# Kernel tuning notes

Measured on AMD Instinct MI355X. Metric: run time of the kernel, lower is better.

Reference implementation:

```python
import jax, jax.numpy as jnp
import numpy as np

B, T, E, H = 2, 2048, 1024, 16
Dh = E // H  # head_size = 64


def setup_inputs() -> dict:
    key = jax.random.key(0)
    ks = jax.random.split(key, 6)
    s = E ** -0.5
    x = jax.random.normal(ks[0], (B, T, E), dtype=jnp.float32)
    Wq = jax.random.normal(ks[1], (H, E, Dh), dtype=jnp.float32) * s
    Wk = jax.random.normal(ks[2], (H, E, Dh), dtype=jnp.float32) * s
    Wv = jax.random.normal(ks[3], (H, E, Dh), dtype=jnp.float32) * s
    wo_w = jax.random.normal(ks[4], (E, E), dtype=jnp.float32) * s  # torch Linear weight [out,in]
    wo_b = jax.random.normal(ks[5], (E,), dtype=jnp.float32) * 0.01
    return {"x": x, "Wq": Wq, "Wk": Wk, "Wv": Wv, "wo_w": wo_w, "wo_b": wo_b}


def reference(x, Wq, Wk, Wv, wo_w, wo_b):
    # Batched equivalent of the per-head Python loop: project all heads at once.
    q = jnp.einsum('bte,hed->bhtd', x, Wq)
    k = jnp.einsum('bte,hed->bhtd', x, Wk)
    v = jnp.einsum('bte,hed->bhtd', x, Wv)
    scale = Dh ** -0.5
    scores = jnp.einsum('bhtd,bhsd->bhts', q, k) * scale  # [B,H,T,T]
    causal = jnp.tril(jnp.ones((T, T), dtype=bool))
    scores = jnp.where(causal, scores, jnp.finfo(scores.dtype).min)
    att = jax.nn.softmax(scores, axis=-1)
    out = jnp.einsum('bhts,bhsd->bhtd', att, v)  # [B,H,T,Dh]
    # concat heads (head order along last dim, matching torch.cat over heads)
    out = out.transpose(0, 2, 1, 3).reshape(B, T, E)
    return out @ wo_w.T + wo_b
```

## Files before the change

kernel.cpp:

```cpp
#include <hip/hip_runtime.h>

#define B_ 2
#define T_ 2048
#define E_ 1024
#define H_ 16
#define DH 64

typedef unsigned short u16;
typedef unsigned int u32;
typedef __bf16 bf16x8 __attribute__((ext_vector_type(8)));
typedef float f32x4 __attribute__((ext_vector_type(4)));

__device__ __forceinline__ u16 f2bf(float f) {
  u32 u = __builtin_bit_cast(u32, f);
  u = u + 0x7FFFu + ((u >> 16) & 1u);
  return (u16)(u >> 16);
}
__device__ __forceinline__ float bf2f(u16 v) {
  return __builtin_bit_cast(float, (u32)v << 16);
}
__device__ __forceinline__ bf16x8 ldfrag(const u16* p) { return *(const bf16x8*)p; }

__device__ __forceinline__ void gload_lds16(const u16* g, u16* l) {
  __builtin_amdgcn_global_load_lds((const __attribute__((address_space(1))) u32*)g,
                                   (__attribute__((address_space(3))) u32*)l, 16, 0, 0);
}

__global__ __launch_bounds__(256) void k_conv_all(const float* __restrict__ x,
                                                  const float* __restrict__ Wq,
                                                  const float* __restrict__ Wk,
                                                  const float* __restrict__ Wv,
                                                  const float* __restrict__ wo_w,
                                                  u16* __restrict__ xb, u16* __restrict__ wT,
                                                  u16* __restrict__ woB) {
  __shared__ __align__(16) u16 Ls[64][68];
  const int t = threadIdx.x;
  const int bx = blockIdx.x;
  if (bx < 2048 || bx >= 2816) {
    const float* src = (bx < 2048) ? x : wo_w;
    u16* dst = (bx < 2048) ? xb : woB;
    u32 i = (((bx < 2048) ? bx : (bx - 2816)) * 256u + t) * 8u;
    float4 a = *(const float4*)(src + i);
    float4 b = *(const float4*)(src + i + 4);
    uint4 v;
    v.x = (u32)f2bf(a.x) | ((u32)f2bf(a.y) << 16);
    v.y = (u32)f2bf(a.z) | ((u32)f2bf(a.w) << 16);
    v.z = (u32)f2bf(b.x) | ((u32)f2bf(b.y) << 16);
    v.w = (u32)f2bf(b.z) | ((u32)f2bf(b.w) << 16);
    *(uint4*)(dst + i) = v;
    return;
  }
  const int idx = bx - 2048;
  const int e0 = (idx & 15) * 64;
  const int h = (idx >> 4) & 15;
  const int which = idx >> 8;
  const float* src = (which == 0) ? Wq : ((which == 1) ? Wk : Wv);
  const float scale = (which == 0) ? 0.18033688011112042f : 1.0f;
#pragma unroll
  for (int p = 0; p < 4; p++) {
    int id2 = p * 256 + t;
    int row = id2 >> 4, ch = id2 & 15;
    float4 v = *(const float4*)(src + ((size_t)h * E_ + e0 + row) * DH + ch * 4);
    uint2 pk;
    pk.x = (u32)f2bf(v.x * scale) | ((u32)f2bf(v.y * scale) << 16);
    pk.y = (u32)f2bf(v.z * scale) | ((u32)f2bf(v.w * scale) << 16);
    *(uint2*)(&Ls[row][ch * 4]) = pk;
  }
  __syncthreads();
  u16* dst = wT + ((size_t)which * H_ + h) * (DH * E_);
#pragma unroll
  for (int p = 0; p < 4; p++) {
    int id2 = p * 256 + t;
    int d = id2 >> 4, ec = id2 & 15;
    uint2 pk;
    pk.x = (u32)Ls[ec * 4 + 0][d] | ((u32)Ls[ec * 4 + 1][d] << 16);
    pk.y = (u32)Ls[ec * 4 + 2][d] | ((u32)Ls[ec * 4 + 3][d] << 16);
    *(uint2*)(dst + (size_t)d * E_ + e0 + ec * 4) = pk;
  }
}

__global__ __launch_bounds__(256, 3) void k_qkv(const u16* __restrict__ xb, const u16* __restrict__ wT,
                                                u16* __restrict__ Qb, u16* __restrict__ Kb,
                                                u16* __restrict__ VbT) {
  __shared__ __align__(16) u16 As[128 * 64];
  __shared__ __align__(16) u16 Bs[128 * 64];
  const int tid = threadIdx.x;
  const int w = tid >> 6, lane = tid & 63, quad = lane >> 4, lr = lane & 15;
  const int wr = w >> 1, wc = w & 1;
  const int t0 = blockIdx.x * 128;
  const int n0 = blockIdx.y * 128;
  const int sr = lane >> 3, sc = lane & 7;

  f32x4 acc[4][4];
  const f32x4 z4 = {0.f, 0.f, 0.f, 0.f};
#pragma unroll
  for (int i = 0; i < 4; i++)
#pragma unroll
    for (int j = 0; j < 4; j++) acc[i][j] = z4;

  for (int k0 = 0; k0 < E_; k0 += 64) {
    __syncthreads();
#pragma unroll
    for (int ii = 0; ii < 4; ii++) {
      int ra = w * 32 + ii * 8 + sr;
      gload_lds16(xb + (size_t)(t0 + ra) * E_ + k0 + ((sc ^ (ra & 7)) << 3),
                  As + (w * 32 + ii * 8) * 64);
      gload_lds16(wT + (size_t)(n0 + ra) * E_ + k0 + ((sc ^ (ra & 7)) << 3),
                  Bs + (w * 32 + ii * 8) * 64);
    }
    __syncthreads();
#pragma unroll
    for (int kk = 0; kk < 2; kk++) {
      bf16x8 af[4], bfv[4];
#pragma unroll
      for (int rt = 0; rt < 4; rt++) {
        int row = wr * 64 + rt * 16 + lr;
        af[rt] = ldfrag(As + row * 64 + (((kk * 4 + quad) ^ (row & 7)) << 3));
      }
#pragma unroll
      for (int ct = 0; ct < 4; ct++) {
        int row = wc * 64 + ct * 16 + lr;
        bfv[ct] = ldfrag(Bs + row * 64 + (((kk * 4 + quad) ^ (row & 7)) << 3));
      }
#pragma unroll
      for (int rt = 0; rt < 4; rt++)
#pragma unroll
        for (int ct = 0; ct < 4; ct++)
          acc[rt][ct] = __builtin_amdgcn_mfma_f32_16x16x32_bf16(af[rt], bfv[ct], acc[rt][ct], 0, 0, 0);
    }
  }

  const int qkv = n0 >> 10;
  if (qkv < 2) {
    u16* outp = (qkv == 0) ? Qb : Kb;
#pragma unroll
    for (int rt = 0; rt < 4; rt++)
#pragma unroll
      for (int ct = 0; ct < 4; ct++) {
        int n = n0 + wc * 64 + ct * 16 + lr;
        int h = (n >> 6) & 15, d = n & 63;
#pragma unroll
        for (int r = 0; r < 4; r++) {
          int t = t0 + wr * 64 + rt * 16 + quad * 4 + r;
          int bb = t >> 11, tt = t & 2047;
          outp[(((size_t)bb * H_ + h) * T_ + tt) * DH + d] = f2bf(acc[rt][ct][r]);
        }
      }
  } else {
#pragma unroll
    for (int rt = 0; rt < 4; rt++)
#pragma unroll
      for (int ct = 0; ct < 4; ct++) {
        int n = n0 + wc * 64 + ct * 16 + lr;
        int h = (n >> 6) & 15, d = n & 63;
        int t = t0 + wr * 64 + rt * 16 + quad * 4;
        int bb = t >> 11, tt = t & 2047;
        uint2 pk;
        pk.x = (u32)f2bf(acc[rt][ct][0]) | ((u32)f2bf(acc[rt][ct][1]) << 16);
        pk.y = (u32)f2bf(acc[rt][ct][2]) | ((u32)f2bf(acc[rt][ct][3]) << 16);
        *(uint2*)(VbT + (((size_t)bb * H_ + h) * DH + d) * T_ + tt) = pk;
      }
  }
}

__global__ __launch_bounds__(256, 6) void k_attn(const u16* __restrict__ Qb, const u16* __restrict__ Kb,
                                                 const u16* __restrict__ VbT, u16* __restrict__ O0,
                                                 u16* __restrict__ O1, u16* __restrict__ O2,
                                                 float* __restrict__ Lb) {
  __shared__ __align__(16) u16 Ks[4096];
  __shared__ __align__(16) u16 Vts[4096];
  __shared__ __align__(16) u16 Ps[4096];
  const int tid = threadIdx.x;
  const int w = tid >> 6, lane = tid & 63, quad = lane >> 4, lr = lane & 15;
  const int l7 = lr & 7;
  const int srow = lane >> 3, schunk = lane & 7;
  const int i = blockIdx.x / 3, s = blockIdx.x - 3 * i;
  const int h = blockIdx.y, bb = blockIdx.z;
  const u16* qb = Qb + ((size_t)bb * H_ + h) * (size_t)(T_ * DH);
  const u16* kb = Kb + ((size_t)bb * H_ + h) * (size_t)(T_ * DH);
  const u16* vbT = VbT + ((size_t)bb * H_ + h) * (size_t)(T_ * DH);
  const f32x4 z4 = {0.f, 0.f, 0.f, 0.f};
  const float MFIX = 20.0f;
  u16* const ops[3] = {O0, O1, O2};

  for (int jb = 0; jb < 2; jb++) {
    const int qt = jb ? i : (31 - i);
    const int t0 = qt * 64;

    const u16* qrow = qb + (size_t)(t0 + w * 16 + lr) * DH;
    bf16x8 bq0 = ldfrag(qrow + quad * 8);
    bf16x8 bq1 = ldfrag(qrow + 32 + quad * 8);

    f32x4 o_acc[4];
#pragma unroll
    for (int dt = 0; dt < 4; dt++) o_acc[dt] = z4;
    float l_i = 0.f;

    for (int jt = s; jt <= qt; jt += 3) {
      const int j0 = jt * 64;
      __syncthreads();
#pragma unroll
      for (int ii = 0; ii < 2; ii++) {
        int r = w * 16 + ii * 8 + srow;
        gload_lds16(kb + (size_t)(j0 + r) * DH + ((schunk ^ (r & 7)) << 3),
                    Ks + (w * 16 + ii * 8) * 64);
        gload_lds16(vbT + (size_t)r * T_ + j0 + ((schunk ^ (r & 7)) << 3),
                    Vts + (w * 16 + ii * 8) * 64);
      }
      __syncthreads();

      f32x4 s_acc[4];
#pragma unroll
      for (int st = 0; st < 4; st++) s_acc[st] = z4;
#pragma unroll
      for (int st = 0; st < 4; st++) {
        bf16x8 ak0 = ldfrag(Ks + (st * 16 + lr) * 64 + ((quad ^ l7) << 3));
        bf16x8 ak1 = ldfrag(Ks + (st * 16 + lr) * 64 + (((4 + quad) ^ l7) << 3));
        s_acc[st] = __builtin_amdgcn_mfma_f32_16x16x32_bf16(ak0, bq0, s_acc[st], 0, 0, 0);
        s_acc[st] = __builtin_amdgcn_mfma_f32_16x16x32_bf16(ak1, bq1, s_acc[st], 0, 0, 0);
      }

      if (jt == qt) {
        int qloc = w * 16 + lr;
#pragma unroll
        for (int st = 0; st < 4; st++) {
          int sbase = st * 16 + quad * 4;
#pragma unroll
          for (int r = 0; r < 4; r++)
            if (sbase + r > qloc) s_acc[st][r] = -__builtin_inff();
        }
      }

      float rsum = 0.f;
#pragma unroll
      for (int st = 0; st < 4; st++) {
        float p0 = __builtin_amdgcn_exp2f(s_acc[st][0] - MFIX);
        float p1 = __builtin_amdgcn_exp2f(s_acc[st][1] - MFIX);
        float p2 = __builtin_amdgcn_exp2f(s_acc[st][2] - MFIX);
        float p3 = __builtin_amdgcn_exp2f(s_acc[st][3] - MFIX);
        rsum += (p0 + p1) + (p2 + p3);
        uint2 pk;
        pk.x = (__builtin_bit_cast(u32, p0) >> 16) | (__builtin_bit_cast(u32, p1) & 0xffff0000u);
        pk.y = (__builtin_bit_cast(u32, p2) >> 16) | (__builtin_bit_cast(u32, p3) & 0xffff0000u);
        *(uint2*)(Ps + (w * 16 + lr) * 64 + (((st * 2 + (quad >> 1)) ^ l7) << 3) + ((quad & 1) << 2)) = pk;
      }
      l_i += rsum;

#pragma unroll
      for (int kk = 0; kk < 2; kk++) {
        bf16x8 bp = ldfrag(Ps + (w * 16 + lr) * 64 + (((kk * 4 + quad) ^ l7) << 3));
#pragma unroll
        for (int dt = 0; dt < 4; dt++) {
          bf16x8 av = ldfrag(Vts + (dt * 16 + lr) * 64 + (((kk * 4 + quad) ^ l7) << 3));
          o_acc[dt] = __builtin_amdgcn_mfma_f32_16x16x32_bf16(av, bp, o_acc[dt], 0, 0, 0);
        }
      }
    }

    l_i += __shfl_xor(l_i, 16);
    l_i += __shfl_xor(l_i, 32);

    u16* op = ops[s];
    int t = t0 + w * 16 + lr;
    u16* orow = op + ((size_t)bb * T_ + t) * E_ + h * DH;
#pragma unroll
    for (int dt = 0; dt < 4; dt++) {
      uint2 pk;
      pk.x = (u32)f2bf(o_acc[dt][0]) | ((u32)f2bf(o_acc[dt][1]) << 16);
      pk.y = (u32)f2bf(o_acc[dt][2]) | ((u32)f2bf(o_acc[dt][3]) << 16);
      *(uint2*)(orow + dt * 16 + quad * 4) = pk;
    }
    if (quad == 0) {
      Lb[((s * B_ + bb) * H_ + h) * T_ + t] = l_i;
    }
  }
}

__global__ void k_combine(const u16* __restrict__ O0, const u16* __restrict__ O1,
                          const u16* __restrict__ O2, const float* __restrict__ Lb,
                          u16* __restrict__ AO) {
  int idx = blockIdx.x * 256 + threadIdx.x;
  int e0 = idx * 8;
  int bb = e0 >> 21, t = (e0 >> 10) & 2047, hh = (e0 >> 6) & 15;
  const int S = B_ * H_ * T_;
  int r = (bb * H_ + hh) * T_ + t;
  float a = 1.0f / (Lb[r] + Lb[r + S] + Lb[r + 2 * S]);
  uint4 u0 = *(const uint4*)(O0 + e0);
  uint4 u1 = *(const uint4*)(O1 + e0);
  uint4 u2 = *(const uint4*)(O2 + e0);
  uint4 o;
  u32 lo, hi;
#define MRG3(a0, a1, a2) (lo = (u32)f2bf((bf2f((u16)(a0)) + bf2f((u16)(a1)) + bf2f((u16)(a2))) * a),  \
                          hi = (u32)f2bf((bf2f((u16)((a0) >> 16)) + bf2f((u16)((a1) >> 16)) +          \
                                          bf2f((u16)((a2) >> 16))) * a),                               \
                          lo | (hi << 16))
  o.x = MRG3(u0.x, u1.x, u2.x);
  o.y = MRG3(u0.y, u1.y, u2.y);
  o.z = MRG3(u0.z, u1.z, u2.z);
  o.w = MRG3(u0.w, u1.w, u2.w);
#undef MRG3
  *(uint4*)(AO + e0) = o;
}

__global__ __launch_bounds__(256, 4) void k_oproj(const u16* __restrict__ AO, const u16* __restrict__ woB,
                                                  const float* __restrict__ bias, float* __restrict__ out) {
  __shared__ __align__(16) u16 As[64 * 64];
  __shared__ __align__(16) u16 Bs[128 * 64];
  const int tid = threadIdx.x;
  const int w = tid >> 6, lane = tid & 63, quad = lane >> 4, lr = lane & 15;
  const int r0 = blockIdx.x * 64, n0 = blockIdx.y * 128;
  const int sr = lane >> 3, sc = lane & 7;

  f32x4 acc[4][2];
  const f32x4 z4 = {0.f, 0.f, 0.f, 0.f};
#pragma unroll
  for (int i = 0; i < 4; i++)
#pragma unroll
    for (int j = 0; j < 2; j++) acc[i][j] = z4;

  for (int k0 = 0; k0 < E_; k0 += 64) {
    __syncthreads();
#pragma unroll
    for (int ii = 0; ii < 2; ii++) {
      int ra = w * 16 + ii * 8 + sr;
      gload_lds16(AO + (size_t)(r0 + ra) * E_ + k0 + ((sc ^ (ra & 7)) << 3),
                  As + (w * 16 + ii * 8) * 64);
    }
#pragma unroll
    for (int ii = 0; ii < 4; ii++) {
      int rb = w * 32 + ii * 8 + sr;
      gload_lds16(woB + (size_t)(n0 + rb) * E_ + k0 + ((sc ^ (rb & 7)) << 3),
                  Bs + (w * 32 + ii * 8) * 64);
    }
    __syncthreads();
#pragma unroll
    for (int kk = 0; kk < 2; kk++) {
      bf16x8 af[4], bfv[2];
#pragma unroll
      for (int rt = 0; rt < 4; rt++) {
        int row = rt * 16 + lr;
        af[rt] = ldfrag(As + row * 64 + (((kk * 4 + quad) ^ (row & 7)) << 3));
      }
#pragma unroll
      for (int ct = 0; ct < 2; ct++) {
        int row = w * 32 + ct * 16 + lr;
        bfv[ct] = ldfrag(Bs + row * 64 + (((kk * 4 + quad) ^ (row & 7)) << 3));
      }
#pragma unroll
      for (int rt = 0; rt < 4; rt++)
#pragma unroll
        for (int ct = 0; ct < 2; ct++)
          acc[rt][ct] = __builtin_amdgcn_mfma_f32_16x16x32_bf16(af[rt], bfv[ct], acc[rt][ct], 0, 0, 0);
    }
  }

#pragma unroll
  for (int ct = 0; ct < 2; ct++) {
    int col = n0 + w * 32 + ct * 16 + lr;
    float bv = bias[col];
#pragma unroll
    for (int rt = 0; rt < 4; rt++)
#pragma unroll
      for (int r = 0; r < 4; r++) {
        int row = r0 + rt * 16 + quad * 4 + r;
        out[(size_t)row * E_ + col] = acc[rt][ct][r] + bv;
      }
  }
}

extern "C" void kernel_launch(void* const* d_in, const int* in_sizes, int n_in,
                              void* d_out, int out_size, void* d_ws, size_t ws_size,
                              hipStream_t stream) {
  const float* x = (const float*)d_in[0];
  const float* Wq = (const float*)d_in[1];
  const float* Wk = (const float*)d_in[2];
  const float* Wv = (const float*)d_in[3];
  const float* wo_w = (const float*)d_in[4];
  const float* wo_b = (const float*)d_in[5];
  float* out = (float*)d_out;
  char* ws = (char*)d_ws;

  u16* xb  = (u16*)(ws + 0);
  u16* wT  = (u16*)(ws + 8388608);
  u16* woB = (u16*)(ws + 14680064);
  u16* Qb  = (u16*)(ws + 16777216);
  u16* Kb  = (u16*)(ws + 25165824);
  u16* VbT = (u16*)(ws + 33554432);
  u16* O0  = (u16*)(ws + 41943040);
  u16* O1  = xb;
  u16* O2  = (u16*)(ws + 50331648);
  u16* AO  = (u16*)(ws + 58720256);
  float* Lb = (float*)(ws + 8388608);

  k_conv_all<<<3328, 256, 0, stream>>>(x, Wq, Wk, Wv, wo_w, xb, wT, woB);
  k_qkv<<<dim3(32, 24), 256, 0, stream>>>(xb, wT, Qb, Kb, VbT);
  k_attn<<<dim3(48, 16, 2), 256, 0, stream>>>(Qb, Kb, VbT, O0, O1, O2, Lb);
  k_combine<<<2048, 256, 0, stream>>>(O0, O1, O2, Lb, AO);
  k_oproj<<<dim3(64, 8), 256, 0, stream>>>(AO, woB, wo_b, out);
}
```

Before: 178.3 us.

## Process two query tiles per attention block and split keys four ways

The attention kernel now handles a 128-row query tile as two 64-row halves that share each loaded K/V tile, which halves K/V global loads per query row. The key-split factor rises from 3 to 4, with a fourth partial output buffer and a combine step that merges four partials. Grid shape and launch bounds change to match. In exchange the kernel uses more registers per thread, targets lower occupancy, and writes one more partial buffer that the combine step must read.

```diff
diff --git a/kernel.cpp b/kernel.cpp
--- a/kernel.cpp
+++ b/kernel.cpp
@@ -163,10 +163,10 @@
   }
 }
 
-__global__ __launch_bounds__(256, 6) void k_attn(const u16* __restrict__ Qb, const u16* __restrict__ Kb,
+__global__ __launch_bounds__(256, 4) void k_attn(const u16* __restrict__ Qb, const u16* __restrict__ Kb,
                                                  const u16* __restrict__ VbT, u16* __restrict__ O0,
                                                  u16* __restrict__ O1, u16* __restrict__ O2,
-                                                 float* __restrict__ Lb) {
+                                                 u16* __restrict__ O3, float* __restrict__ Lb) {
   __shared__ __align__(16) u16 Ks[4096];
   __shared__ __align__(16) u16 Vts[4096];
   __shared__ __align__(16) u16 Ps[4096];
@@ -174,29 +174,34 @@
   const int w = tid >> 6, lane = tid & 63, quad = lane >> 4, lr = lane & 15;
   const int l7 = lr & 7;
   const int srow = lane >> 3, schunk = lane & 7;
-  const int i = blockIdx.x / 3, s = blockIdx.x - 3 * i;
+  const int i = blockIdx.x >> 2, s = blockIdx.x & 3;
   const int h = blockIdx.y, bb = blockIdx.z;
   const u16* qb = Qb + ((size_t)bb * H_ + h) * (size_t)(T_ * DH);
   const u16* kb = Kb + ((size_t)bb * H_ + h) * (size_t)(T_ * DH);
   const u16* vbT = VbT + ((size_t)bb * H_ + h) * (size_t)(T_ * DH);
   const f32x4 z4 = {0.f, 0.f, 0.f, 0.f};
   const float MFIX = 20.0f;
-  u16* const ops[3] = {O0, O1, O2};
+  u16* const ops[4] = {O0, O1, O2, O3};
+  u16* const op = ops[s];
 
   for (int jb = 0; jb < 2; jb++) {
-    const int qt = jb ? i : (31 - i);
-    const int t0 = qt * 64;
-
-    const u16* qrow = qb + (size_t)(t0 + w * 16 + lr) * DH;
-    bf16x8 bq0 = ldfrag(qrow + quad * 8);
-    bf16x8 bq1 = ldfrag(qrow + 32 + quad * 8);
-
-    f32x4 o_acc[4];
-#pragma unroll
-    for (int dt = 0; dt < 4; dt++) o_acc[dt] = z4;
-    float l_i = 0.f;
-
-    for (int jt = s; jt <= qt; jt += 3) {
+    const int qt = jb ? i : (15 - i);
+    const int t0 = qt * 128;
+
+    const u16* qrowA = qb + (size_t)(t0 + w * 16 + lr) * DH;
+    const u16* qrowB = qrowA + (size_t)64 * DH;
+    bf16x8 bqA0 = ldfrag(qrowA + quad * 8);
+    bf16x8 bqA1 = ldfrag(qrowA + 32 + quad * 8);
+    bf16x8 bqB0 = ldfrag(qrowB + quad * 8);
+    bf16x8 bqB1 = ldfrag(qrowB + 32 + quad * 8);
+
+    f32x4 oA[4], oB[4];
+#pragma unroll
+    for (int dt = 0; dt < 4; dt++) { oA[dt] = z4; oB[dt] = z4; }
+    float lA = 0.f, lB = 0.f;
+
+    const int jmax = 2 * qt + 1;
+    for (int jt = s; jt <= jmax; jt += 4) {
       const int j0 = jt * 64;
       __syncthreads();
 #pragma unroll
@@ -209,96 +214,150 @@
       }
       __syncthreads();
 
-      f32x4 s_acc[4];
-#pragma unroll
-      for (int st = 0; st < 4; st++) s_acc[st] = z4;
-#pragma unroll
-      for (int st = 0; st < 4; st++) {
-        bf16x8 ak0 = ldfrag(Ks + (st * 16 + lr) * 64 + ((quad ^ l7) << 3));
-        bf16x8 ak1 = ldfrag(Ks + (st * 16 + lr) * 64 + (((4 + quad) ^ l7) << 3));
-        s_acc[st] = __builtin_amdgcn_mfma_f32_16x16x32_bf16(ak0, bq0, s_acc[st], 0, 0, 0);
-        s_acc[st] = __builtin_amdgcn_mfma_f32_16x16x32_bf16(ak1, bq1, s_acc[st], 0, 0, 0);
-      }
-
-      if (jt == qt) {
-        int qloc = w * 16 + lr;
+      if (jt <= 2 * qt) {
+        f32x4 s_acc[4];
+#pragma unroll
+        for (int st = 0; st < 4; st++) s_acc[st] = z4;
 #pragma unroll
         for (int st = 0; st < 4; st++) {
-          int sbase = st * 16 + quad * 4;
-#pragma unroll
-          for (int r = 0; r < 4; r++)
-            if (sbase + r > qloc) s_acc[st][r] = -__builtin_inff();
-        }
-      }
-
-      float rsum = 0.f;
-#pragma unroll
-      for (int st = 0; st < 4; st++) {
-        float p0 = __builtin_amdgcn_exp2f(s_acc[st][0] - MFIX);
-        float p1 = __builtin_amdgcn_exp2f(s_acc[st][1] - MFIX);
-        float p2 = __builtin_amdgcn_exp2f(s_acc[st][2] - MFIX);
-        float p3 = __builtin_amdgcn_exp2f(s_acc[st][3] - MFIX);
-        rsum += (p0 + p1) + (p2 + p3);
-        uint2 pk;
-        pk.x = (__builtin_bit_cast(u32, p0) >> 16) | (__builtin_bit_cast(u32, p1) & 0xffff0000u);
-        pk.y = (__builtin_bit_cast(u32, p2) >> 16) | (__builtin_bit_cast(u32, p3) & 0xffff0000u);
-        *(uint2*)(Ps + (w * 16 + lr) * 64 + (((st * 2 + (quad >> 1)) ^ l7) << 3) + ((quad & 1) << 2)) = pk;
-      }
-      l_i += rsum;
-
-#pragma unroll
-      for (int kk = 0; kk < 2; kk++) {
-        bf16x8 bp = ldfrag(Ps + (w * 16 + lr) * 64 + (((kk * 4 + quad) ^ l7) << 3));
-#pragma unroll
-        for (int dt = 0; dt < 4; dt++) {
-          bf16x8 av = ldfrag(Vts + (dt * 16 + lr) * 64 + (((kk * 4 + quad) ^ l7) << 3));
-          o_acc[dt] = __builtin_amdgcn_mfma_f32_16x16x32_bf16(av, bp, o_acc[dt], 0, 0, 0);
-        }
-      }
-    }
-
-    l_i += __shfl_xor(l_i, 16);
-    l_i += __shfl_xor(l_i, 32);
-
-    u16* op = ops[s];
-    int t = t0 + w * 16 + lr;
-    u16* orow = op + ((size_t)bb * T_ + t) * E_ + h * DH;
+          bf16x8 ak0 = ldfrag(Ks + (st * 16 + lr) * 64 + ((quad ^ l7) << 3));
+          bf16x8 ak1 = ldfrag(Ks + (st * 16 + lr) * 64 + (((4 + quad) ^ l7) << 3));
+          s_acc[st] = __builtin_amdgcn_mfma_f32_16x16x32_bf16(ak0, bqA0, s_acc[st], 0, 0, 0);
+          s_acc[st] = __builtin_amdgcn_mfma_f32_16x16x32_bf16(ak1, bqA1, s_acc[st], 0, 0, 0);
+        }
+        if (jt == 2 * qt) {
+          int qloc = w * 16 + lr;
+#pragma unroll
+          for (int st = 0; st < 4; st++) {
+            int sbase = st * 16 + quad * 4;
+#pragma unroll
+            for (int r = 0; r < 4; r++)
+              if (sbase + r > qloc) s_acc[st][r] = -__builtin_inff();
+          }
+        }
+        float rsum = 0.f;
+#pragma unroll
+        for (int st = 0; st < 4; st++) {
+          float p0 = __builtin_amdgcn_exp2f(s_acc[st][0] - MFIX);
+          float p1 = __builtin_amdgcn_exp2f(s_acc[st][1] - MFIX);
+          float p2 = __builtin_amdgcn_exp2f(s_acc[st][2] - MFIX);
+          float p3 = __builtin_amdgcn_exp2f(s_acc[st][3] - MFIX);
+          rsum += (p0 + p1) + (p2 + p3);
+          uint2 pk;
+          pk.x = (__builtin_bit_cast(u32, p0) >> 16) | (__builtin_bit_cast(u32, p1) & 0xffff0000u);
+          pk.y = (__builtin_bit_cast(u32, p2) >> 16) | (__builtin_bit_cast(u32, p3) & 0xffff0000u);
+          *(uint2*)(Ps + (w * 16 + lr) * 64 + (((st * 2 + (quad >> 1)) ^ l7) << 3) + ((quad & 1) << 2)) = pk;
+        }
+        lA += rsum;
+#pragma unroll
+        for (int kk = 0; kk < 2; kk++) {
+          bf16x8 bp = ldfrag(Ps + (w * 16 + lr) * 64 + (((kk * 4 + quad) ^ l7) << 3));
+#pragma unroll
+          for (int dt = 0; dt < 4; dt++) {
+            bf16x8 av = ldfrag(Vts + (dt * 16 + lr) * 64 + (((kk * 4 + quad) ^ l7) << 3));
+            oA[dt] = __builtin_amdgcn_mfma_f32_16x16x32_bf16(av, bp, oA[dt], 0, 0, 0);
+          }
+        }
+      }
+
+      {
+        f32x4 s_acc[4];
+#pragma unroll
+        for (int st = 0; st < 4; st++) s_acc[st] = z4;
+#pragma unroll
+        for (int st = 0; st < 4; st++) {
+          bf16x8 ak0 = ldfrag(Ks + (st * 16 + lr) * 64 + ((quad ^ l7) << 3));
+          bf16x8 ak1 = ldfrag(Ks + (st * 16 + lr) * 64 + (((4 + quad) ^ l7) << 3));
+          s_acc[st] = __builtin_amdgcn_mfma_f32_16x16x32_bf16(ak0, bqB0, s_acc[st], 0, 0, 0);
+          s_acc[st] = __builtin_amdgcn_mfma_f32_16x16x32_bf16(ak1, bqB1, s_acc[st], 0, 0, 0);
+        }
+        if (jt == jmax) {
+          int qloc = w * 16 + lr;
+#pragma unroll
+          for (int st = 0; st < 4; st++) {
+            int sbase = st * 16 + quad * 4;
+#pragma unroll
+            for (int r = 0; r < 4; r++)
+              if (sbase + r > qloc) s_acc[st][r] = -__builtin_inff();
+          }
+        }
+        float rsum = 0.f;
+#pragma unroll
+        for (int st = 0; st < 4; st++) {
+          float p0 = __builtin_amdgcn_exp2f(s_acc[st][0] - MFIX);
+          float p1 = __builtin_amdgcn_exp2f(s_acc[st][1] - MFIX);
+          float p2 = __builtin_amdgcn_exp2f(s_acc[st][2] - MFIX);
+          float p3 = __builtin_amdgcn_exp2f(s_acc[st][3] - MFIX);
+          rsum += (p0 + p1) + (p2 + p3);
+          uint2 pk;
+          pk.x = (__builtin_bit_cast(u32, p0) >> 16) | (__builtin_bit_cast(u32, p1) & 0xffff0000u);
+          pk.y = (__builtin_bit_cast(u32, p2) >> 16) | (__builtin_bit_cast(u32, p3) & 0xffff0000u);
+          *(uint2*)(Ps + (w * 16 + lr) * 64 + (((st * 2 + (quad >> 1)) ^ l7) << 3) + ((quad & 1) << 2)) = pk;
+        }
+        lB += rsum;
+#pragma unroll
+        for (int kk = 0; kk < 2; kk++) {
+          bf16x8 bp = ldfrag(Ps + (w * 16 + lr) * 64 + (((kk * 4 + quad) ^ l7) << 3));
+#pragma unroll
+          for (int dt = 0; dt < 4; dt++) {
+            bf16x8 av = ldfrag(Vts + (dt * 16 + lr) * 64 + (((kk * 4 + quad) ^ l7) << 3));
+            oB[dt] = __builtin_amdgcn_mfma_f32_16x16x32_bf16(av, bp, oB[dt], 0, 0, 0);
+          }
+        }
+      }
+    }
+
+    lA += __shfl_xor(lA, 16);
+    lA += __shfl_xor(lA, 32);
+    lB += __shfl_xor(lB, 16);
+    lB += __shfl_xor(lB, 32);
+
+    int tA = t0 + w * 16 + lr;
+    u16* orowA = op + ((size_t)bb * T_ + tA) * E_ + h * DH;
+    u16* orowB = orowA + (size_t)64 * E_;
 #pragma unroll
     for (int dt = 0; dt < 4; dt++) {
-      uint2 pk;
-      pk.x = (u32)f2bf(o_acc[dt][0]) | ((u32)f2bf(o_acc[dt][1]) << 16);
-      pk.y = (u32)f2bf(o_acc[dt][2]) | ((u32)f2bf(o_acc[dt][3]) << 16);
-      *(uint2*)(orow + dt * 16 + quad * 4) = pk;
+      uint2 pkA, pkB;
+      pkA.x = (u32)f2bf(oA[dt][0]) | ((u32)f2bf(oA[dt][1]) << 16);
+      pkA.y = (u32)f2bf(oA[dt][2]) | ((u32)f2bf(oA[dt][3]) << 16);
+      pkB.x = (u32)f2bf(oB[dt][0]) | ((u32)f2bf(oB[dt][1]) << 16);
+      pkB.y = (u32)f2bf(oB[dt][2]) | ((u32)f2bf(oB[dt][3]) << 16);
+      *(uint2*)(orowA + dt * 16 + quad * 4) = pkA;
+      *(uint2*)(orowB + dt * 16 + quad * 4) = pkB;
     }
     if (quad == 0) {
-      Lb[((s * B_ + bb) * H_ + h) * T_ + t] = l_i;
+      int base = ((s * B_ + bb) * H_ + h) * T_;
+      Lb[base + tA] = lA;
+      Lb[base + tA + 64] = lB;
     }
   }
 }
 
 __global__ void k_combine(const u16* __restrict__ O0, const u16* __restrict__ O1,
-                          const u16* __restrict__ O2, const float* __restrict__ Lb,
-                          u16* __restrict__ AO) {
+                          const u16* __restrict__ O2, const u16* __restrict__ O3,
+                          const float* __restrict__ Lb, u16* __restrict__ AO) {
   int idx = blockIdx.x * 256 + threadIdx.x;
   int e0 = idx * 8;
   int bb = e0 >> 21, t = (e0 >> 10) & 2047, hh = (e0 >> 6) & 15;
   const int S = B_ * H_ * T_;
   int r = (bb * H_ + hh) * T_ + t;
-  float a = 1.0f / (Lb[r] + Lb[r + S] + Lb[r + 2 * S]);
+  float a = 1.0f / (Lb[r] + Lb[r + S] + Lb[r + 2 * S] + Lb[r + 3 * S]);
   uint4 u0 = *(const uint4*)(O0 + e0);
   uint4 u1 = *(const uint4*)(O1 + e0);
   uint4 u2 = *(const uint4*)(O2 + e0);
+  uint4 u3 = *(const uint4*)(O3 + e0);
   uint4 o;
   u32 lo, hi;
-#define MRG3(a0, a1, a2) (lo = (u32)f2bf((bf2f((u16)(a0)) + bf2f((u16)(a1)) + bf2f((u16)(a2))) * a),  \
-                          hi = (u32)f2bf((bf2f((u16)((a0) >> 16)) + bf2f((u16)((a1) >> 16)) +          \
-                                          bf2f((u16)((a2) >> 16))) * a),                               \
-                          lo | (hi << 16))
-  o.x = MRG3(u0.x, u1.x, u2.x);
-  o.y = MRG3(u0.y, u1.y, u2.y);
-  o.z = MRG3(u0.z, u1.z, u2.z);
-  o.w = MRG3(u0.w, u1.w, u2.w);
-#undef MRG3
+#define MRG4(a0, a1, a2, a3)                                                                      \
+  (lo = (u32)f2bf((bf2f((u16)(a0)) + bf2f((u16)(a1)) + bf2f((u16)(a2)) + bf2f((u16)(a3))) * a),   \
+   hi = (u32)f2bf((bf2f((u16)((a0) >> 16)) + bf2f((u16)((a1) >> 16)) + bf2f((u16)((a2) >> 16)) +  \
+                   bf2f((u16)((a3) >> 16))) * a),                                                 \
+   lo | (hi << 16))
+  o.x = MRG4(u0.x, u1.x, u2.x, u3.x);
+  o.y = MRG4(u0.y, u1.y, u2.y, u3.y);
+  o.z = MRG4(u0.z, u1.z, u2.z, u3.z);
+  o.w = MRG4(u0.w, u1.w, u2.w, u3.w);
+#undef MRG4
   *(uint4*)(AO + e0) = o;
 }
 
@@ -390,11 +449,12 @@
   u16* O1  = xb;
   u16* O2  = (u16*)(ws + 50331648);
   u16* AO  = (u16*)(ws + 58720256);
+  u16* O3  = (u16*)(ws + 67108864);
   float* Lb = (float*)(ws + 8388608);
 
   k_conv_all<<<3328, 256, 0, stream>>>(x, Wq, Wk, Wv, wo_w, xb, wT, woB);
   k_qkv<<<dim3(32, 24), 256, 0, stream>>>(xb, wT, Qb, Kb, VbT);
-  k_attn<<<dim3(48, 16, 2), 256, 0, stream>>>(Qb, Kb, VbT, O0, O1, O2, Lb);
-  k_combine<<<2048, 256, 0, stream>>>(O0, O1, O2, Lb, AO);
+  k_attn<<<dim3(32, 16, 2), 256, 0, stream>>>(Qb, Kb, VbT, O0, O1, O2, O3, Lb);
+  k_combine<<<2048, 256, 0, stream>>>(O0, O1, O2, O3, Lb, AO);
   k_oproj<<<dim3(64, 8), 256, 0, stream>>>(AO, woB, wo_b, out);
 }
```

Result: faster. 174.1 us (-2.4%).

## Drop split-KV attention and combine kernel; shrink o-proj tile to 64x64

Applied to the files above, without the earlier changes.

Attention no longer splits the key range three ways. Each block now walks all key tiles for its paired query tiles and normalizes by the row sum in its epilogue, writing the final attention output directly. This removes the k_combine kernel and three partial output buffers, but the grid drops from 1536 to 512 blocks, with longer serial loops and less parallelism on a large-CU GPU. The output projection tile also shrinks from 64x128 to 64x64, doubling the block count to fill more CUs at the cost of less operand reuse.

```diff
diff --git a/kernel.cpp b/kernel.cpp
--- a/kernel.cpp
+++ b/kernel.cpp
@@ -15,9 +15,6 @@
   u32 u = __builtin_bit_cast(u32, f);
   u = u + 0x7FFFu + ((u >> 16) & 1u);
   return (u16)(u >> 16);
-}
-__device__ __forceinline__ float bf2f(u16 v) {
-  return __builtin_bit_cast(float, (u32)v << 16);
 }
 __device__ __forceinline__ bf16x8 ldfrag(const u16* p) { return *(const bf16x8*)p; }
 
@@ -163,10 +160,8 @@
   }
 }
 
-__global__ __launch_bounds__(256, 6) void k_attn(const u16* __restrict__ Qb, const u16* __restrict__ Kb,
-                                                 const u16* __restrict__ VbT, u16* __restrict__ O0,
-                                                 u16* __restrict__ O1, u16* __restrict__ O2,
-                                                 float* __restrict__ Lb) {
+__global__ __launch_bounds__(256, 4) void k_attn(const u16* __restrict__ Qb, const u16* __restrict__ Kb,
+                                                 const u16* __restrict__ VbT, u16* __restrict__ AO) {
   __shared__ __align__(16) u16 Ks[4096];
   __shared__ __align__(16) u16 Vts[4096];
   __shared__ __align__(16) u16 Ps[4096];
@@ -174,14 +169,13 @@
   const int w = tid >> 6, lane = tid & 63, quad = lane >> 4, lr = lane & 15;
   const int l7 = lr & 7;
   const int srow = lane >> 3, schunk = lane & 7;
-  const int i = blockIdx.x / 3, s = blockIdx.x - 3 * i;
+  const int i = blockIdx.x;
   const int h = blockIdx.y, bb = blockIdx.z;
   const u16* qb = Qb + ((size_t)bb * H_ + h) * (size_t)(T_ * DH);
   const u16* kb = Kb + ((size_t)bb * H_ + h) * (size_t)(T_ * DH);
   const u16* vbT = VbT + ((size_t)bb * H_ + h) * (size_t)(T_ * DH);
   const f32x4 z4 = {0.f, 0.f, 0.f, 0.f};
   const float MFIX = 20.0f;
-  u16* const ops[3] = {O0, O1, O2};
 
   for (int jb = 0; jb < 2; jb++) {
     const int qt = jb ? i : (31 - i);
@@ -196,7 +190,7 @@
     for (int dt = 0; dt < 4; dt++) o_acc[dt] = z4;
     float l_i = 0.f;
 
-    for (int jt = s; jt <= qt; jt += 3) {
+    for (int jt = 0; jt <= qt; jt++) {
       const int j0 = jt * 64;
       __syncthreads();
 #pragma unroll
@@ -259,64 +253,32 @@
 
     l_i += __shfl_xor(l_i, 16);
     l_i += __shfl_xor(l_i, 32);
-
-    u16* op = ops[s];
+    float inv = 1.0f / l_i;
     int t = t0 + w * 16 + lr;
-    u16* orow = op + ((size_t)bb * T_ + t) * E_ + h * DH;
+    u16* orow = AO + ((size_t)bb * T_ + t) * E_ + h * DH;
 #pragma unroll
     for (int dt = 0; dt < 4; dt++) {
       uint2 pk;
-      pk.x = (u32)f2bf(o_acc[dt][0]) | ((u32)f2bf(o_acc[dt][1]) << 16);
-      pk.y = (u32)f2bf(o_acc[dt][2]) | ((u32)f2bf(o_acc[dt][3]) << 16);
+      pk.x = (u32)f2bf(o_acc[dt][0] * inv) | ((u32)f2bf(o_acc[dt][1] * inv) << 16);
+      pk.y = (u32)f2bf(o_acc[dt][2] * inv) | ((u32)f2bf(o_acc[dt][3] * inv) << 16);
       *(uint2*)(orow + dt * 16 + quad * 4) = pk;
     }
-    if (quad == 0) {
-      Lb[((s * B_ + bb) * H_ + h) * T_ + t] = l_i;
-    }
-  }
-}
-
-__global__ void k_combine(const u16* __restrict__ O0, const u16* __restrict__ O1,
-                          const u16* __restrict__ O2, const float* __restrict__ Lb,
-                          u16* __restrict__ AO) {
-  int idx = blockIdx.x * 256 + threadIdx.x;
-  int e0 = idx * 8;
-  int bb = e0 >> 21, t = (e0 >> 10) & 2047, hh = (e0 >> 6) & 15;
-  const int S = B_ * H_ * T_;
-  int r = (bb * H_ + hh) * T_ + t;
-  float a = 1.0f / (Lb[r] + Lb[r + S] + Lb[r + 2 * S]);
-  uint4 u0 = *(const uint4*)(O0 + e0);
-  uint4 u1 = *(const uint4*)(O1 + e0);
-  uint4 u2 = *(const uint4*)(O2 + e0);
-  uint4 o;
-  u32 lo, hi;
-#define MRG3(a0, a1, a2) (lo = (u32)f2bf((bf2f((u16)(a0)) + bf2f((u16)(a1)) + bf2f((u16)(a2))) * a),  \
-                          hi = (u32)f2bf((bf2f((u16)((a0) >> 16)) + bf2f((u16)((a1) >> 16)) +          \
-                                          bf2f((u16)((a2) >> 16))) * a),                               \
-                          lo | (hi << 16))
-  o.x = MRG3(u0.x, u1.x, u2.x);
-  o.y = MRG3(u0.y, u1.y, u2.y);
-  o.z = MRG3(u0.z, u1.z, u2.z);
-  o.w = MRG3(u0.w, u1.w, u2.w);
-#undef MRG3
-  *(uint4*)(AO + e0) = o;
+  }
 }
 
 __global__ __launch_bounds__(256, 4) void k_oproj(const u16* __restrict__ AO, const u16* __restrict__ woB,
                                                   const float* __restrict__ bias, float* __restrict__ out) {
   __shared__ __align__(16) u16 As[64 * 64];
-  __shared__ __align__(16) u16 Bs[128 * 64];
+  __shared__ __align__(16) u16 Bs[64 * 64];
   const int tid = threadIdx.x;
   const int w = tid >> 6, lane = tid & 63, quad = lane >> 4, lr = lane & 15;
-  const int r0 = blockIdx.x * 64, n0 = blockIdx.y * 128;
+  const int r0 = blockIdx.x * 64, n0 = blockIdx.y * 64;
   const int sr = lane >> 3, sc = lane & 7;
 
-  f32x4 acc[4][2];
+  f32x4 acc[4];
   const f32x4 z4 = {0.f, 0.f, 0.f, 0.f};
 #pragma unroll
-  for (int i = 0; i < 4; i++)
-#pragma unroll
-    for (int j = 0; j < 2; j++) acc[i][j] = z4;
+  for (int i = 0; i < 4; i++) acc[i] = z4;
 
   for (int k0 = 0; k0 < E_; k0 += 64) {
     __syncthreads();
@@ -325,45 +287,37 @@
       int ra = w * 16 + ii * 8 + sr;
       gload_lds16(AO + (size_t)(r0 + ra) * E_ + k0 + ((sc ^ (ra & 7)) << 3),
                   As + (w * 16 + ii * 8) * 64);
-    }
-#pragma unroll
-    for (int ii = 0; ii < 4; ii++) {
-      int rb = w * 32 + ii * 8 + sr;
-      gload_lds16(woB + (size_t)(n0 + rb) * E_ + k0 + ((sc ^ (rb & 7)) << 3),
-                  Bs + (w * 32 + ii * 8) * 64);
+      gload_lds16(woB + (size_t)(n0 + ra) * E_ + k0 + ((sc ^ (ra & 7)) << 3),
+                  Bs + (w * 16 + ii * 8) * 64);
     }
     __syncthreads();
 #pragma unroll
     for (int kk = 0; kk < 2; kk++) {
-      bf16x8 af[4], bfv[2];
+      bf16x8 af[4], bfv;
 #pragma unroll
       for (int rt = 0; rt < 4; rt++) {
         int row = rt * 16 + lr;
         af[rt] = ldfrag(As + row * 64 + (((kk * 4 + quad) ^ (row & 7)) << 3));
       }
-#pragma unroll
-      for (int ct = 0; ct < 2; ct++) {
-        int row = w * 32 + ct * 16 + lr;
-        bfv[ct] = ldfrag(Bs + row * 64 + (((kk * 4 + quad) ^ (row & 7)) << 3));
+      {
+        int row = w * 16 + lr;
+        bfv = ldfrag(Bs + row * 64 + (((kk * 4 + quad) ^ (row & 7)) << 3));
       }
 #pragma unroll
       for (int rt = 0; rt < 4; rt++)
-#pragma unroll
-        for (int ct = 0; ct < 2; ct++)
-          acc[rt][ct] = __builtin_amdgcn_mfma_f32_16x16x32_bf16(af[rt], bfv[ct], acc[rt][ct], 0, 0, 0);
-    }
-  }
-
-#pragma unroll
-  for (int ct = 0; ct < 2; ct++) {
-    int col = n0 + w * 32 + ct * 16 + lr;
+        acc[rt] = __builtin_amdgcn_mfma_f32_16x16x32_bf16(af[rt], bfv, acc[rt], 0, 0, 0);
+    }
+  }
+
+  {
+    int col = n0 + w * 16 + lr;
     float bv = bias[col];
 #pragma unroll
     for (int rt = 0; rt < 4; rt++)
 #pragma unroll
       for (int r = 0; r < 4; r++) {
         int row = r0 + rt * 16 + quad * 4 + r;
-        out[(size_t)row * E_ + col] = acc[rt][ct][r] + bv;
+        out[(size_t)row * E_ + col] = acc[rt][r] + bv;
       }
   }
 }
@@ -386,15 +340,10 @@
   u16* Qb  = (u16*)(ws + 16777216);
   u16* Kb  = (u16*)(ws + 25165824);
   u16* VbT = (u16*)(ws + 33554432);
-  u16* O0  = (u16*)(ws + 41943040);
-  u16* O1  = xb;
-  u16* O2  = (u16*)(ws + 50331648);
-  u16* AO  = (u16*)(ws + 58720256);
-  float* Lb = (float*)(ws + 8388608);
+  u16* AO  = (u16*)(ws + 41943040);
 
   k_conv_all<<<3328, 256, 0, stream>>>(x, Wq, Wk, Wv, wo_w, xb, wT, woB);
   k_qkv<<<dim3(32, 24), 256, 0, stream>>>(xb, wT, Qb, Kb, VbT);
-  k_attn<<<dim3(48, 16, 2), 256, 0, stream>>>(Qb, Kb, VbT, O0, O1, O2, Lb);
-  k_combine<<<2048, 256, 0, stream>>>(O0, O1, O2, Lb, AO);
-  k_oproj<<<dim3(64, 8), 256, 0, stream>>>(AO, woB, wo_b, out);
-}
+  k_attn<<<dim3(16, 16, 2), 256, 0, stream>>>(Qb, Kb, VbT, AO);
+  k_oproj<<<dim3(64, 16), 256, 0, stream>>>(AO, woB, wo_b, out);
+}
```

Result: faster. 173.8 us (-2.5%).
